# Performance work log

Measured on AMD Instinct MI355X. Metric: run time of the kernel, lower is better.

Reference implementation:

```python
import jax, jax.numpy as jnp
import numpy as np

DATA_SZ = 1000   # number of timesteps, from source: data_sz = 1000
BATCH = 1024
DIM = 64
HIDDEN = 256


def setup_inputs() -> dict:
    key = jax.random.key(0)
    k0, k1, k2, k3, k4 = jax.random.split(key, 5)
    y0 = jax.random.normal(k0, (BATCH, DIM), dtype=jnp.float32)
    t = jnp.linspace(0.0, 15.0, DATA_SZ).astype(jnp.float32)
    W1 = jax.random.normal(k1, (DIM, HIDDEN), dtype=jnp.float32) * (1.0 / np.sqrt(DIM))
    b1 = jax.random.normal(k2, (HIDDEN,), dtype=jnp.float32) * 0.01
    W2 = jax.random.normal(k3, (HIDDEN, DIM), dtype=jnp.float32) * (1.0 / np.sqrt(HIDDEN))
    b2 = jax.random.normal(k4, (DIM,), dtype=jnp.float32) * 0.01
    return {"y0": y0, "t": t, "W1": W1, "b1": b1, "W2": W2, "b2": b2}


def reference(y0, t, W1, b1, W2, b2):
    # func: autonomous tanh-MLP vector field f(t, y) = tanh(y@W1+b1)@W2+b2
    def func(ti, y):
        return jnp.tanh(y @ W1 + b1) @ W2 + b2

    # solver: classic RK4 step returning dy (matches solver(func, t0, h, y0) -> dy)
    def rk4_dy(t0, h, y):
        half = h * 0.5
        k1 = func(t0, y)
        k2 = func(t0 + half, y + half * k1)
        k3 = func(t0 + half, y + half * k2)
        k4 = func(t0 + h, y + h * k3)
        return (h / 6.0) * (k1 + 2.0 * k2 + 2.0 * k3 + k4)

    ts = t[:-1]
    hs = t[1:] - t[:-1]

    def step(y, th):
        t0, h = th
        y1 = y + rk4_dy(t0, h, y)
        return y1, y1

    _, ys = jax.lax.scan(step, y0, (ts, hs))  # ys: [T-1, B, D]
    return jnp.concatenate([y0[None], ys], axis=0)  # [T, B, D]
```

## Files before the change

kernel.cpp:

```cpp
#include <hip/hip_runtime.h>


typedef _Float16 h8 __attribute__((ext_vector_type(8)));
typedef float f4 __attribute__((ext_vector_type(4)));

#define NB 1024
#define ND 64
#define NH 256
#define RPB 16
#define NBLK 64
#define NTHR 512
#define LO_SC 2048.0f
#define LO_ISC 4.8828125e-4f

#define MFMA16(A, B, C) __builtin_amdgcn_mfma_f32_16x16x32_f16((A), (B), (C), 0, 0, 0)
#define PIN(X) asm volatile("" : "+v"(X))

#define BSYNC() do { \
    asm volatile("s_waitcnt lgkmcnt(0)" ::: "memory"); \
    __builtin_amdgcn_s_barrier(); \
    asm volatile("" ::: "memory"); \
} while (0)

__device__ __forceinline__ float fast_tanh(float x) {
    float e = __expf(2.0f * x);
    float r = __builtin_amdgcn_rcpf(e + 1.0f);
    return 1.0f - 2.0f * r;
}

__global__ __launch_bounds__(NTHR, 2)
void node_rk4_mfma(const float* __restrict__ y0,
                   const float* __restrict__ t,
                   const float* __restrict__ W1,
                   const float* __restrict__ b1,
                   const float* __restrict__ W2,
                   const float* __restrict__ b2,
                   float* __restrict__ out, int nsteps)
{
    __shared__ __align__(16) _Float16 xPh[2][64][8], xPl[2][64][8];
    __shared__ __align__(16) _Float16 aPh[8][64][8], aPl[8][64][8];

    const int tid = threadIdx.x;
    const int w  = tid >> 6, l = tid & 63;
    const int ln = l & 15,  lg = l >> 4;

    if (w < 4) {
        h8 WH0,WH1,WH2,WH3,WH4,WH5,WH6,WH7;
        h8 WL0,WL1,WL2,WL3,WL4,WL5,WL6,WL7;
#define LG1(NT,KT,H,L) { \
        int n_ = (w<<6) + ((NT)<<4) + ln; \
        int kb_ = (KT)*32 + lg*8; \
        _Pragma("unroll") for (int j=0;j<8;++j) { \
            float f_ = W1[(kb_+j)*NH + n_]; \
            _Float16 fh_ = (_Float16)f_; \
            H[j] = fh_; L[j] = (_Float16)((f_-(float)fh_)*LO_SC); } }
        LG1(0,0,WH0,WL0) LG1(0,1,WH1,WL1)
        LG1(1,0,WH2,WL2) LG1(1,1,WH3,WL3)
        LG1(2,0,WH4,WL4) LG1(2,1,WH5,WL5)
        LG1(3,0,WH6,WL6) LG1(3,1,WH7,WL7)
        PIN(WH0);PIN(WH1);PIN(WH2);PIN(WH3);PIN(WH4);PIN(WH5);PIN(WH6);PIN(WH7);
        PIN(WL0);PIN(WL1);PIN(WL2);PIN(WL3);PIN(WL4);PIN(WL5);PIN(WL6);PIN(WL7);
        const float bv0 = b1[(w<<6) +  0 + ln];
        const float bv1 = b1[(w<<6) + 16 + ln];
        const float bv2 = b1[(w<<6) + 32 + ln];
        const float bv3 = b1[(w<<6) + 48 + ln];

        _Float16 *aph0,*aph1,*aph2,*aph3, *apl0,*apl1,*apl2,*apl3;
#define SPTR(NT, PH, PL) { \
        int n_ = (w<<6) + ((NT)<<4) + ln; \
        int kt_ = n_>>5, g_ = (n_>>3)&3, j_ = n_&7; \
        PH = &aPh[kt_][(g_<<4)+lg*4][j_]; \
        PL = &aPl[kt_][(g_<<4)+lg*4][j_]; }
        SPTR(0,aph0,apl0) SPTR(1,aph1,apl1) SPTR(2,aph2,apl2) SPTR(3,aph3,apl3)
        const h8* xp0h = (const h8*)&xPh[0][l][0];
        const h8* xp1h = (const h8*)&xPh[1][l][0];
        const h8* xp0l = (const h8*)&xPl[0][l][0];
        const h8* xp1l = (const h8*)&xPl[1][l][0];

        BSYNC();
        const int nevals = 4 * nsteps;
        for (int e = 0; e < nevals; ++e) {
            h8 xh0 = *xp0h, xh1 = *xp1h, xl0 = *xp0l, xl1 = *xp1l;
            f4 zz = {0.f, 0.f, 0.f, 0.f};
#define G1NT(PH, PL, HH0, HH1, LL0, LL1, BV) { \
            f4 aH = {BV,BV,BV,BV}; \
            aH = MFMA16(xh0, HH0, aH);  aH = MFMA16(xh1, HH1, aH); \
            f4 aL1 = MFMA16(xl0, HH0, zz); aL1 = MFMA16(xl1, HH1, aL1); \
            f4 aL2 = MFMA16(xh0, LL0, zz); aL2 = MFMA16(xh1, LL1, aL2); \
            f4 hv = aH + LO_ISC*(aL1 + aL2); \
            _Pragma("unroll") for (int r=0;r<4;++r) { \
                float a_ = fast_tanh(hv[r]); \
                _Float16 ah_ = (_Float16)a_; \
                PH[r*8] = ah_; \
                PL[r*8] = (_Float16)((a_-(float)ah_)*LO_SC); } }
            G1NT(aph0, apl0, WH0, WH1, WL0, WL1, bv0)
            G1NT(aph1, apl1, WH2, WH3, WL2, WL3, bv1)
            G1NT(aph2, apl2, WH4, WH5, WL4, WL5, bv2)
            G1NT(aph3, apl3, WH6, WH7, WL6, WL7, bv3)
            BSYNC();
            BSYNC();
        }
    } else {
        const int g2 = w - 4;
        const int d  = (g2<<4) + ln;
        h8 VH0,VH1,VH2,VH3,VH4,VH5,VH6,VH7;
        h8 VL0,VL1,VL2,VL3,VL4,VL5,VL6,VL7;
#define LG2(KT,H,L) { \
        int kb_ = (KT)*32 + lg*8; \
        _Pragma("unroll") for (int j=0;j<8;++j) { \
            float f_ = W2[(kb_+j)*ND + d]; \
            _Float16 fh_ = (_Float16)f_; \
            H[j] = fh_; L[j] = (_Float16)((f_-(float)fh_)*LO_SC); } }
        LG2(0,VH0,VL0) LG2(1,VH1,VL1) LG2(2,VH2,VL2) LG2(3,VH3,VL3)
        LG2(4,VH4,VL4) LG2(5,VH5,VL5) LG2(6,VH6,VL6) LG2(7,VH7,VL7)
        PIN(VH0);PIN(VH1);PIN(VH2);PIN(VH3);PIN(VH4);PIN(VH5);PIN(VH6);PIN(VH7);
        PIN(VL0);PIN(VL1);PIN(VL2);PIN(VL3);PIN(VL4);PIN(VL5);PIN(VL6);PIN(VL7);
        const float b2v = b2[d];

        const h8 *pa0 = (const h8*)&aPh[0][l][0], *pa1 = (const h8*)&aPh[1][l][0];
        const h8 *pa2 = (const h8*)&aPh[2][l][0], *pa3 = (const h8*)&aPh[3][l][0];
        const h8 *pa4 = (const h8*)&aPh[4][l][0], *pa5 = (const h8*)&aPh[5][l][0];
        const h8 *pa6 = (const h8*)&aPh[6][l][0], *pa7 = (const h8*)&aPh[7][l][0];
        const h8 *pc0 = (const h8*)&aPl[0][l][0], *pc1 = (const h8*)&aPl[1][l][0];
        const h8 *pc2 = (const h8*)&aPl[2][l][0], *pc3 = (const h8*)&aPl[3][l][0];
        const h8 *pc4 = (const h8*)&aPl[4][l][0], *pc5 = (const h8*)&aPl[5][l][0];
        const h8 *pc6 = (const h8*)&aPl[6][l][0], *pc7 = (const h8*)&aPl[7][l][0];

        const size_t rb = (size_t)blockIdx.x * RPB * ND;
        f4 ys, ka;
        #pragma unroll
        for (int r=0;r<4;++r) {
            float v = y0[rb + (size_t)(4*lg+r)*ND + d];
            ys[r] = v;
            out[rb + (size_t)(4*lg+r)*ND + d] = v;
        }
        const int xkt = g2 >> 1;
        const int xg  = 2*(g2&1) + (ln>>3);
        const int xj  = ln & 7;
        _Float16* xph = &xPh[xkt][(xg<<4)+lg*4][xj];
        _Float16* xpl = &xPl[xkt][(xg<<4)+lg*4][xj];
#define PACKX(XV, R) { \
        float xv_ = (XV); \
        _Float16 xh_ = (_Float16)xv_; \
        xph[(R)*8] = xh_; \
        xpl[(R)*8] = (_Float16)((xv_-(float)xh_)*LO_SC); }
        #pragma unroll
        for (int r=0;r<4;++r) PACKX(ys[r], r)
        BSYNC();

        for (int s = 0; s < nsteps; ++s) {
            float dt = t[s+1] - t[s];
            size_t ob = (size_t)(s+1)*(NB*ND) + rb;
#define G2EVAL(ST) { \
            BSYNC();   \
            h8 a0=*pa0,a1=*pa1,a2=*pa2,a3=*pa3,a4=*pa4,a5=*pa5,a6=*pa6,a7=*pa7; \
            h8 c0=*pc0,c1=*pc1,c2=*pc2,c3=*pc3,c4=*pc4,c5=*pc5,c6=*pc6,c7=*pc7; \
            f4 zz = {0.f,0.f,0.f,0.f}; \
            f4 HA=MFMA16(a0,VH0,zz), HB=MFMA16(a1,VH1,zz); \
            f4 HC=MFMA16(a2,VH2,zz), HD=MFMA16(a3,VH3,zz); \
            HA=MFMA16(a4,VH4,HA); HB=MFMA16(a5,VH5,HB); \
            HC=MFMA16(a6,VH6,HC); HD=MFMA16(a7,VH7,HD); \
            f4 LA=MFMA16(c0,VH0,zz), LB=MFMA16(c1,VH1,zz); \
            f4 LC=MFMA16(c2,VH2,zz), LD=MFMA16(c3,VH3,zz); \
            LA=MFMA16(c4,VH4,LA); LB=MFMA16(c5,VH5,LB); \
            LC=MFMA16(c6,VH6,LC); LD=MFMA16(c7,VH7,LD); \
            f4 MA=MFMA16(a0,VL0,zz), MB=MFMA16(a1,VL1,zz); \
            f4 MC=MFMA16(a2,VL2,zz), MD=MFMA16(a3,VL3,zz); \
            MA=MFMA16(a4,VL4,MA); MB=MFMA16(a5,VL5,MB); \
            MC=MFMA16(a6,VL6,MC); MD=MFMA16(a7,VL7,MD); \
            f4 kv = ((HA+HB)+(HC+HD)) \
                  + LO_ISC*(((LA+LB)+(LC+LD)) + ((MA+MB)+(MC+MD))); \
            _Pragma("unroll") for (int r=0;r<4;++r) kv[r] += b2v; \
            f4 xn; \
            if ((ST)==1)      { ka = kv;        xn = ys + (0.5f*dt)*kv; } \
            else if ((ST)==2) { ka += 2.0f*kv;  xn = ys + (0.5f*dt)*kv; } \
            else if ((ST)==3) { ka += 2.0f*kv;  xn = ys + dt*kv; } \
            else { ys = ys + (dt*(1.0f/6.0f))*(ka + kv); xn = ys; \
                   _Pragma("unroll") for (int r=0;r<4;++r) \
                       out[ob + (size_t)(4*lg+r)*ND + d] = ys[r]; } \
            _Pragma("unroll") for (int r=0;r<4;++r) PACKX(xn[r], r) \
            BSYNC();   }
            G2EVAL(1)
            G2EVAL(2)
            G2EVAL(3)
            G2EVAL(4)
        }
    }
}

extern "C" void kernel_launch(void* const* d_in, const int* in_sizes, int n_in,
                              void* d_out, int out_size, void* d_ws, size_t ws_size,
                              hipStream_t stream) {
    const float* y0 = (const float*)d_in[0];
    const float* t  = (const float*)d_in[1];
    const float* W1 = (const float*)d_in[2];
    const float* b1 = (const float*)d_in[3];
    const float* W2 = (const float*)d_in[4];
    const float* b2 = (const float*)d_in[5];
    float* out = (float*)d_out;
    int nsteps = in_sizes[1] - 1;
    hipLaunchKernelGGL(node_rk4_mfma, dim3(NBLK), dim3(NTHR), 0, stream,
                       y0, t, W1, b1, W2, b2, out, nsteps);
}
```

Before: 5.099 ms.

## Interleave two row chunks per block to pipeline the two MLP layers

Each block now handles 32 rows as two 16-row chunks and uses 32 blocks. The first-layer waves compute one chunk while the second-layer waves process the other, with double-buffered shared memory for both x and activations. Before, the two wave groups alternated and each sat idle during the other's phase; now each barrier interval does useful work on both sides. The trade-off is half as many blocks, so fewer CUs are busy, and twice the sequential work per block.

```diff
diff --git a/kernel.cpp b/kernel.cpp
--- a/kernel.cpp
+++ b/kernel.cpp
@@ -7,8 +7,8 @@
 #define NB 1024
 #define ND 64
 #define NH 256
-#define RPB 16
-#define NBLK 64
+#define RPB 32
+#define NBLK 32
 #define NTHR 512
 #define LO_SC 2048.0f
 #define LO_ISC 4.8828125e-4f
@@ -37,8 +37,8 @@
                    const float* __restrict__ b2,
                    float* __restrict__ out, int nsteps)
 {
-    __shared__ __align__(16) _Float16 xPh[2][64][8], xPl[2][64][8];
-    __shared__ __align__(16) _Float16 aPh[8][64][8], aPl[8][64][8];
+    __shared__ __align__(16) _Float16 xPh[2][2][64][8], xPl[2][2][64][8];
+    __shared__ __align__(16) _Float16 aPh[2][8][64][8], aPl[2][8][64][8];
 
     const int tid = threadIdx.x;
     const int w  = tid >> 6, l = tid & 63;
@@ -69,20 +69,15 @@
 #define SPTR(NT, PH, PL) { \
         int n_ = (w<<6) + ((NT)<<4) + ln; \
         int kt_ = n_>>5, g_ = (n_>>3)&3, j_ = n_&7; \
-        PH = &aPh[kt_][(g_<<4)+lg*4][j_]; \
-        PL = &aPl[kt_][(g_<<4)+lg*4][j_]; }
+        PH = &aPh[0][kt_][(g_<<4)+lg*4][j_]; \
+        PL = &aPl[0][kt_][(g_<<4)+lg*4][j_]; }
         SPTR(0,aph0,apl0) SPTR(1,aph1,apl1) SPTR(2,aph2,apl2) SPTR(3,aph3,apl3)
-        const h8* xp0h = (const h8*)&xPh[0][l][0];
-        const h8* xp1h = (const h8*)&xPh[1][l][0];
-        const h8* xp0l = (const h8*)&xPl[0][l][0];
-        const h8* xp1l = (const h8*)&xPl[1][l][0];
-
-        BSYNC();
-        const int nevals = 4 * nsteps;
-        for (int e = 0; e < nevals; ++e) {
-            h8 xh0 = *xp0h, xh1 = *xp1h, xl0 = *xp0l, xl1 = *xp1l;
-            f4 zz = {0.f, 0.f, 0.f, 0.f};
-#define G1NT(PH, PL, HH0, HH1, LL0, LL1, BV) { \
+        const h8* xp0h = (const h8*)&xPh[0][0][l][0];
+        const h8* xp1h = (const h8*)&xPh[0][1][l][0];
+        const h8* xp0l = (const h8*)&xPl[0][0][l][0];
+        const h8* xp1l = (const h8*)&xPl[0][1][l][0];
+
+#define G1NT(C, PH, PL, HH0, HH1, LL0, LL1, BV) { \
             f4 aH = {BV,BV,BV,BV}; \
             aH = MFMA16(xh0, HH0, aH);  aH = MFMA16(xh1, HH1, aH); \
             f4 aL1 = MFMA16(xl0, HH0, zz); aL1 = MFMA16(xl1, HH1, aL1); \
@@ -91,15 +86,25 @@
             _Pragma("unroll") for (int r=0;r<4;++r) { \
                 float a_ = fast_tanh(hv[r]); \
                 _Float16 ah_ = (_Float16)a_; \
-                PH[r*8] = ah_; \
-                PL[r*8] = (_Float16)((a_-(float)ah_)*LO_SC); } }
-            G1NT(aph0, apl0, WH0, WH1, WL0, WL1, bv0)
-            G1NT(aph1, apl1, WH2, WH3, WL2, WL3, bv1)
-            G1NT(aph2, apl2, WH4, WH5, WL4, WL5, bv2)
-            G1NT(aph3, apl3, WH6, WH7, WL6, WL7, bv3)
-            BSYNC();
-            BSYNC();
+                PH[(C)*4096 + r*8] = ah_; \
+                PL[(C)*4096 + r*8] = (_Float16)((a_-(float)ah_)*LO_SC); } }
+#define G1SLOT(C) { \
+            h8 xh0 = xp0h[(C)*128], xh1 = xp1h[(C)*128]; \
+            h8 xl0 = xp0l[(C)*128], xl1 = xp1l[(C)*128]; \
+            f4 zz = {0.f,0.f,0.f,0.f}; \
+            G1NT(C, aph0, apl0, WH0, WH1, WL0, WL1, bv0) \
+            G1NT(C, aph1, apl1, WH2, WH3, WL2, WL3, bv1) \
+            G1NT(C, aph2, apl2, WH4, WH5, WL4, WL5, bv2) \
+            G1NT(C, aph3, apl3, WH6, WH7, WL6, WL7, bv3) }
+
+        BSYNC();
+        for (int s = 0; s < nsteps; ++s) {
+            G1SLOT(0) BSYNC(); G1SLOT(1) BSYNC();
+            G1SLOT(0) BSYNC(); G1SLOT(1) BSYNC();
+            G1SLOT(0) BSYNC(); G1SLOT(1) BSYNC();
+            G1SLOT(0) BSYNC(); G1SLOT(1) BSYNC();
         }
+        BSYNC();
     } else {
         const int g2 = w - 4;
         const int d  = (g2<<4) + ln;
@@ -117,44 +122,47 @@
         PIN(VL0);PIN(VL1);PIN(VL2);PIN(VL3);PIN(VL4);PIN(VL5);PIN(VL6);PIN(VL7);
         const float b2v = b2[d];
 
-        const h8 *pa0 = (const h8*)&aPh[0][l][0], *pa1 = (const h8*)&aPh[1][l][0];
-        const h8 *pa2 = (const h8*)&aPh[2][l][0], *pa3 = (const h8*)&aPh[3][l][0];
-        const h8 *pa4 = (const h8*)&aPh[4][l][0], *pa5 = (const h8*)&aPh[5][l][0];
-        const h8 *pa6 = (const h8*)&aPh[6][l][0], *pa7 = (const h8*)&aPh[7][l][0];
-        const h8 *pc0 = (const h8*)&aPl[0][l][0], *pc1 = (const h8*)&aPl[1][l][0];
-        const h8 *pc2 = (const h8*)&aPl[2][l][0], *pc3 = (const h8*)&aPl[3][l][0];
-        const h8 *pc4 = (const h8*)&aPl[4][l][0], *pc5 = (const h8*)&aPl[5][l][0];
-        const h8 *pc6 = (const h8*)&aPl[6][l][0], *pc7 = (const h8*)&aPl[7][l][0];
+        const h8 *pa0 = (const h8*)&aPh[0][0][l][0], *pa1 = (const h8*)&aPh[0][1][l][0];
+        const h8 *pa2 = (const h8*)&aPh[0][2][l][0], *pa3 = (const h8*)&aPh[0][3][l][0];
+        const h8 *pa4 = (const h8*)&aPh[0][4][l][0], *pa5 = (const h8*)&aPh[0][5][l][0];
+        const h8 *pa6 = (const h8*)&aPh[0][6][l][0], *pa7 = (const h8*)&aPh[0][7][l][0];
+        const h8 *pc0 = (const h8*)&aPl[0][0][l][0], *pc1 = (const h8*)&aPl[0][1][l][0];
+        const h8 *pc2 = (const h8*)&aPl[0][2][l][0], *pc3 = (const h8*)&aPl[0][3][l][0];
+        const h8 *pc4 = (const h8*)&aPl[0][4][l][0], *pc5 = (const h8*)&aPl[0][5][l][0];
+        const h8 *pc6 = (const h8*)&aPl[0][6][l][0], *pc7 = (const h8*)&aPl[0][7][l][0];
 
         const size_t rb = (size_t)blockIdx.x * RPB * ND;
-        f4 ys, ka;
+        f4 ys0, ka0, ys1, ka1;
         #pragma unroll
         for (int r=0;r<4;++r) {
-            float v = y0[rb + (size_t)(4*lg+r)*ND + d];
-            ys[r] = v;
-            out[rb + (size_t)(4*lg+r)*ND + d] = v;
+            float v0 = y0[rb + (size_t)(4*lg+r)*ND + d];
+            ys0[r] = v0; out[rb + (size_t)(4*lg+r)*ND + d] = v0;
+            float v1 = y0[rb + (size_t)(16+4*lg+r)*ND + d];
+            ys1[r] = v1; out[rb + (size_t)(16+4*lg+r)*ND + d] = v1;
         }
         const int xkt = g2 >> 1;
         const int xg  = 2*(g2&1) + (ln>>3);
         const int xj  = ln & 7;
-        _Float16* xph = &xPh[xkt][(xg<<4)+lg*4][xj];
-        _Float16* xpl = &xPl[xkt][(xg<<4)+lg*4][xj];
-#define PACKX(XV, R) { \
+        _Float16* xph = &xPh[0][xkt][(xg<<4)+lg*4][xj];
+        _Float16* xpl = &xPl[0][xkt][(xg<<4)+lg*4][xj];
+#define PACKX(C, XV, R) { \
         float xv_ = (XV); \
         _Float16 xh_ = (_Float16)xv_; \
-        xph[(R)*8] = xh_; \
-        xpl[(R)*8] = (_Float16)((xv_-(float)xh_)*LO_SC); }
+        xph[(C)*1024 + (R)*8] = xh_; \
+        xpl[(C)*1024 + (R)*8] = (_Float16)((xv_-(float)xh_)*LO_SC); }
         #pragma unroll
-        for (int r=0;r<4;++r) PACKX(ys[r], r)
+        for (int r=0;r<4;++r) { PACKX(0, ys0[r], r) PACKX(1, ys1[r], r) }
+        BSYNC();
         BSYNC();
 
         for (int s = 0; s < nsteps; ++s) {
             float dt = t[s+1] - t[s];
             size_t ob = (size_t)(s+1)*(NB*ND) + rb;
-#define G2EVAL(ST) { \
-            BSYNC();   \
-            h8 a0=*pa0,a1=*pa1,a2=*pa2,a3=*pa3,a4=*pa4,a5=*pa5,a6=*pa6,a7=*pa7; \
-            h8 c0=*pc0,c1=*pc1,c2=*pc2,c3=*pc3,c4=*pc4,c5=*pc5,c6=*pc6,c7=*pc7; \
+#define G2EVAL(C, ST) { \
+            h8 a0=pa0[(C)*512],a1=pa1[(C)*512],a2=pa2[(C)*512],a3=pa3[(C)*512]; \
+            h8 a4=pa4[(C)*512],a5=pa5[(C)*512],a6=pa6[(C)*512],a7=pa7[(C)*512]; \
+            h8 c0=pc0[(C)*512],c1=pc1[(C)*512],c2=pc2[(C)*512],c3=pc3[(C)*512]; \
+            h8 c4=pc4[(C)*512],c5=pc5[(C)*512],c6=pc6[(C)*512],c7=pc7[(C)*512]; \
             f4 zz = {0.f,0.f,0.f,0.f}; \
             f4 HA=MFMA16(a0,VH0,zz), HB=MFMA16(a1,VH1,zz); \
             f4 HC=MFMA16(a2,VH2,zz), HD=MFMA16(a3,VH3,zz); \
@@ -172,18 +180,17 @@
                   + LO_ISC*(((LA+LB)+(LC+LD)) + ((MA+MB)+(MC+MD))); \
             _Pragma("unroll") for (int r=0;r<4;++r) kv[r] += b2v; \
             f4 xn; \
-            if ((ST)==1)      { ka = kv;        xn = ys + (0.5f*dt)*kv; } \
-            else if ((ST)==2) { ka += 2.0f*kv;  xn = ys + (0.5f*dt)*kv; } \
-            else if ((ST)==3) { ka += 2.0f*kv;  xn = ys + dt*kv; } \
-            else { ys = ys + (dt*(1.0f/6.0f))*(ka + kv); xn = ys; \
+            if ((ST)==1)      { ka##C = kv;        xn = ys##C + (0.5f*dt)*kv; } \
+            else if ((ST)==2) { ka##C += 2.0f*kv;  xn = ys##C + (0.5f*dt)*kv; } \
+            else if ((ST)==3) { ka##C += 2.0f*kv;  xn = ys##C + dt*kv; } \
+            else { ys##C = ys##C + (dt*(1.0f/6.0f))*(ka##C + kv); xn = ys##C; \
                    _Pragma("unroll") for (int r=0;r<4;++r) \
-                       out[ob + (size_t)(4*lg+r)*ND + d] = ys[r]; } \
-            _Pragma("unroll") for (int r=0;r<4;++r) PACKX(xn[r], r) \
-            BSYNC();   }
-            G2EVAL(1)
-            G2EVAL(2)
-            G2EVAL(3)
-            G2EVAL(4)
+                       out[ob + (size_t)((C)*16 + 4*lg+r)*ND + d] = ys##C[r]; } \
+            _Pragma("unroll") for (int r=0;r<4;++r) PACKX(C, xn[r], r) }
+            G2EVAL(0,1) BSYNC(); G2EVAL(1,1) BSYNC();
+            G2EVAL(0,2) BSYNC(); G2EVAL(1,2) BSYNC();
+            G2EVAL(0,3) BSYNC(); G2EVAL(1,3) BSYNC();
+            G2EVAL(0,4) BSYNC(); G2EVAL(1,4) BSYNC();
         }
     }
 }
```

Measured after the change: 7.871 ms. 1.54x slower.
